# Kernel optimization log

Measured on AMD Instinct MI355X. Metric: run time of the kernel, lower is better.

The kernel has to match this reference:

```python
import jax, jax.numpy as jnp
import numpy as np

B, C, W, H = 2, 64, 96, 96  # N = W*H = 9216 spatial positions


def conv1x1(x, w, b):
    # x: (B, Cin, W, H), w: (Cout, Cin), b: (Cout,) -> (B, Cout, W, H)
    return jnp.einsum('bchw,oc->bohw', x, w) + b[None, :, None, None]


def setup_inputs() -> dict:
    key = jax.random.key(0)
    ks = jax.random.split(key, 4)
    c8 = C // 8
    s = 0.05  # small weight scale keeps softmax logits in a sane range
    return {
        'x': jax.random.normal(ks[0], (B, C, W, H), jnp.float32),
        'wq': jax.random.normal(ks[1], (c8, C), jnp.float32) * s,
        'bq': jnp.zeros((c8,), jnp.float32),
        'wk': jax.random.normal(ks[2], (c8, C), jnp.float32) * s,
        'bk': jnp.zeros((c8,), jnp.float32),
        'wv': jax.random.normal(ks[3], (C, C), jnp.float32) * s,
        'bv': jnp.zeros((C,), jnp.float32),
        'gamma': jnp.full((1,), 0.5, jnp.float32),
    }


def reference(x, wq, bq, wk, bk, wv, bv, gamma):
    b, c, w, h = x.shape
    n = w * h
    q = conv1x1(x, wq, bq).reshape(b, -1, n)   # (B, C//8, N)
    k = conv1x1(x, wk, bk).reshape(b, -1, n)   # (B, C//8, N)
    v = conv1x1(x, wv, bv).reshape(b, c, n)    # (B, C, N)
    energy = jnp.einsum('bci,bcj->bij', q, k)  # (B, N, N)
    attn = jax.nn.softmax(energy, axis=-1)
    # torch.bmm(v, attn): out[b,c,i] = sum_j v[b,c,j] * attn[b,j,i]
    out = jnp.einsum('bcj,bji->bci', v, attn).reshape(b, c, w, h)
    return gamma * out + x
```

## Files before the change

### kernel.cpp

```cpp
#include <hip/hip_runtime.h>

using half2v  = __attribute__((ext_vector_type(2))) _Float16;
using half4   = __attribute__((ext_vector_type(4))) _Float16;
using half8   = __attribute__((ext_vector_type(8))) _Float16;
using floatx4 = __attribute__((ext_vector_type(4))) float;

constexpr int BATCH = 2;
constexpr int NPOS  = 96 * 96;
constexpr int NT    = NPOS / 16;
constexpr int NST   = NPOS / 32;

#define EXP2(x) __builtin_amdgcn_exp2f(x)

__device__ inline half8 p8_of(floatx4 e0, floatx4 e1) {
    half2v a0 = __builtin_bit_cast(half2v,
        __builtin_amdgcn_cvt_pkrtz(EXP2(e0[0]), EXP2(e0[1])));
    half2v a1 = __builtin_bit_cast(half2v,
        __builtin_amdgcn_cvt_pkrtz(EXP2(e0[2]), EXP2(e0[3])));
    half2v a2 = __builtin_bit_cast(half2v,
        __builtin_amdgcn_cvt_pkrtz(EXP2(e1[0]), EXP2(e1[1])));
    half2v a3 = __builtin_bit_cast(half2v,
        __builtin_amdgcn_cvt_pkrtz(EXP2(e1[2]), EXP2(e1[3])));
    half8 p = {a0[0], a0[1], a1[0], a1[1], a2[0], a2[1], a3[0], a3[1]};
    return p;
}

__global__ __launch_bounds__(256) void qkv_kernel(
    const float* __restrict__ x,
    const float* __restrict__ wq, const float* __restrict__ bq,
    const float* __restrict__ wk, const float* __restrict__ bk,
    const float* __restrict__ wv, const float* __restrict__ bv,
    _Float16* __restrict__ Qf, _Float16* __restrict__ Kf,
    _Float16* __restrict__ Vf)
{
    __shared__ float W[80][64];
    __shared__ float bias[80];
    __shared__ float qs[32][8];
    __shared__ float ks[32][8];
    __shared__ _Float16 vs[32][64];
    const int tid = threadIdx.x;
    for (int idx = tid; idx < 80 * 64; idx += 256) {
        int o = idx >> 6, c = idx & 63;
        float w;
        if (o < 8)       w = wq[o * 64 + c];
        else if (o < 16) w = wk[(o - 8) * 64 + c];
        else             w = wv[(o - 16) * 64 + c];
        W[o][c] = w;
    }
    if (tid < 80) {
        float bb;
        if (tid < 8)       bb = bq[tid];
        else if (tid < 16) bb = bk[tid - 8];
        else               bb = bv[tid - 16];
        bias[tid] = bb;
    }
    __syncthreads();

    const int js = blockIdx.x;
    const int b  = blockIdx.y;
    const int part = tid >> 5;
    const int jl   = tid & 31;
    const int i    = js * 32 + jl;

    float xr[64];
    #pragma unroll
    for (int c = 0; c < 64; ++c)
        xr[c] = x[(size_t)(b * 64 + c) * NPOS + i];

    #pragma unroll
    for (int q = 0; q < 10; ++q) {
        const int o = part * 10 + q;
        float s = bias[o];
        #pragma unroll
        for (int c4 = 0; c4 < 16; ++c4) {
            float4 w4 = *(const float4*)&W[o][c4 * 4];
            s += w4.x * xr[c4*4+0] + w4.y * xr[c4*4+1]
               + w4.z * xr[c4*4+2] + w4.w * xr[c4*4+3];
        }
        if (o < 8)       qs[jl][o] = s;
        else if (o < 16) ks[jl][o - 8] = s;
        else             vs[jl][o - 16] = (_Float16)s;
    }
    __syncthreads();

    const size_t tile = (size_t)b * NST + js;
    {
        const int ct = tid >> 6, l = tid & 63;
        const int g = l >> 4, cl = l & 15;
        half8 o8;
        #pragma unroll
        for (int idx = 0; idx < 8; ++idx)
            o8[idx] = vs[8 * g + idx][16 * ct + cl];
        *(half8*)&Vf[(tile * 256 + ct * 64 + l) * 8] = o8;
    }
    if (tid < 128) {
        const int l = tid >> 1, e = tid & 1;
        const int m = l & 15, g = l >> 4;
        const int jsrc = 8 * (m >> 2) + 4 * e + (m & 3);
        constexpr float LOG2E = 1.44269504088896f;
        half4 qh;
        #pragma unroll
        for (int r = 0; r < 4; ++r)
            qh[r] = (g < 2) ? (_Float16)(qs[jsrc][4 * g + r] * LOG2E)
                            : (_Float16)0.f;
        ((half4*)Qf)[(tile * 64 + l) * 2 + e] = qh;
    } else {
        const int t = tid - 128;
        const int ht = t >> 6, l = t & 63;
        const int il = l & 15, g = l >> 4;
        const int it = js * 2 + ht;
        half4 kh;
        #pragma unroll
        for (int r = 0; r < 4; ++r) {
            if (g < 2)       kh[r] = (_Float16)ks[16 * ht + il][4 * g + r];
            else if (g == 2) kh[r] = (r < 2) ? (_Float16)1.f : (_Float16)0.f;
            else             kh[r] = (_Float16)0.f;
        }
        ((half4*)Kf)[(size_t)(b * NT + it) * 64 + l] = kh;
    }
}

__global__ __launch_bounds__(256, 4) void denom_kernel(
    const _Float16* __restrict__ Qf, const _Float16* __restrict__ Kf,
    float* __restrict__ Lp)
{
    __shared__ float LpS[4][64];
    const int tid = threadIdx.x;
    const int w = tid >> 6, l = tid & 63;
    const int jgl = blockIdx.x;
    const int b   = blockIdx.y;
    const int ih  = blockIdx.z;
    const half8* __restrict__ qfb = (const half8*)Qf + (size_t)b * NST * 64;
    const half4* __restrict__ kfb = (const half4*)Kf + (size_t)b * NT * 64;

    half8 qvA = qfb[(size_t)(jgl * 2 + 0) * 64 + l];
    half8 qvB = qfb[(size_t)(jgl * 2 + 1) * 64 + l];
    half4 q0 = __builtin_shufflevector(qvA, qvA, 0, 1, 2, 3);
    half4 q1 = __builtin_shufflevector(qvA, qvA, 4, 5, 6, 7);
    half4 q2 = __builtin_shufflevector(qvB, qvB, 0, 1, 2, 3);
    half4 q3 = __builtin_shufflevector(qvB, qvB, 4, 5, 6, 7);

    float sum[4][4];
    #pragma unroll
    for (int s = 0; s < 4; ++s)
        #pragma unroll
        for (int r = 0; r < 4; ++r) sum[s][r] = 0.f;

    #define DSTEP(KF) do { \
        floatx4 z = {0.f,0.f,0.f,0.f}; \
        floatx4 e0 = __builtin_amdgcn_mfma_f32_16x16x16f16(q0, KF, z, 0,0,0); \
        floatx4 e1 = __builtin_amdgcn_mfma_f32_16x16x16f16(q1, KF, z, 0,0,0); \
        floatx4 e2 = __builtin_amdgcn_mfma_f32_16x16x16f16(q2, KF, z, 0,0,0); \
        floatx4 e3 = __builtin_amdgcn_mfma_f32_16x16x16f16(q3, KF, z, 0,0,0); \
        _Pragma("unroll") \
        for (int r = 0; r < 4; ++r) { \
            sum[0][r] += EXP2(e0[r]); sum[1][r] += EXP2(e1[r]); \
            sum[2][r] += EXP2(e2[r]); sum[3][r] += EXP2(e3[r]); } \
    } while (0)

    const half4* kp = kfb + (size_t)(ih * (NT/2) + w) * 64 + l;
    half4 kf = *kp;
    for (int k = 0; k < 71; ++k) {
        kp += 256;
        half4 kn = *kp;
        DSTEP(kf);
        kf = kn;
    }
    DSTEP(kf);
    #undef DSTEP

    #pragma unroll
    for (int s = 0; s < 4; ++s)
        #pragma unroll
        for (int r = 0; r < 4; ++r)
            #pragma unroll
            for (int m = 1; m < 16; m <<= 1)
                sum[s][r] += __shfl_xor(sum[s][r], m, 64);

    if ((l & 15) == 0) {
        const int g = l >> 4;
        #pragma unroll
        for (int s = 0; s < 4; ++s)
            #pragma unroll
            for (int r = 0; r < 4; ++r)
                LpS[w][(s >> 1) * 32 + 8 * g + 4 * (s & 1) + r] = sum[s][r];
    }
    __syncthreads();
    if (tid < 64) {
        float tot = LpS[0][tid] + LpS[1][tid] + LpS[2][tid] + LpS[3][tid];
        Lp[((size_t)ih * BATCH + b) * NPOS + jgl * 64 + tid] = tot;
    }
}

__global__ __launch_bounds__(256) void patch_kernel(
    const float* __restrict__ Lp, _Float16* __restrict__ Qf)
{
    const int idx = blockIdx.x * 256 + threadIdx.x;
    const int b = idx / NPOS;
    const int j = idx - b * NPOS;
    const float L = Lp[(size_t)b * NPOS + j] + Lp[(size_t)(BATCH + b) * NPOS + j];
    const float v = -__log2f(L);
    _Float16 hi = (_Float16)v;
    _Float16 lo = (_Float16)(v - (float)hi);
    const int js = j >> 5, off = j & 31;
    const int m = ((off >> 3) << 2) | (off & 3);
    const int e = (off >> 2) & 1;
    const size_t tile = (size_t)b * NST + js;
    half2v hl = {hi, lo};
    ((half2v*)Qf)[((tile * 64 + m + 32) * 2 + e) * 2] = hl;
}

__global__ __launch_bounds__(256, 3) void attn_kernel(
    const _Float16* __restrict__ Qf, const _Float16* __restrict__ Kf,
    const _Float16* __restrict__ Vf,
    const float* __restrict__ x, const float* __restrict__ gamma,
    float* __restrict__ out)
{
    __shared__ float red[4][3][64][9];
    const int s = blockIdx.x;
    const int xcd = s & 7;
    const int b   = xcd >> 2;
    const int r2  = (s >> 3) * 4 + (xcd & 3);
    const int igl = r2 % 192;
    const int ch  = r2 / 192;
    const int tid = threadIdx.x;
    const int w = tid >> 6, l = tid & 63;
    const int it0 = igl * 3, i0 = igl * 48;

    const half8* __restrict__ qfb = (const half8*)Qf + (size_t)b * NST * 64;
    const half4* __restrict__ kfb = (const half4*)Kf + (size_t)b * NT * 64;
    const half8* __restrict__ vfb = (const half8*)Vf + (size_t)b * NST * 256;

    half4 kf[3];
    #pragma unroll
    for (int st = 0; st < 3; ++st) kf[st] = kfb[(size_t)(it0 + st) * 64 + l];

    floatx4 acc[3][2];
    #pragma unroll
    for (int st = 0; st < 3; ++st) {
        acc[st][0] = (floatx4){0.f, 0.f, 0.f, 0.f};
        acc[st][1] = (floatx4){0.f, 0.f, 0.f, 0.f};
    }

    #define ASTEP(QV, V0, V1) do { \
        half4 qe0 = __builtin_shufflevector(QV, QV, 0, 1, 2, 3); \
        half4 qe1 = __builtin_shufflevector(QV, QV, 4, 5, 6, 7); \
        floatx4 z = {0.f,0.f,0.f,0.f}; \
        _Pragma("unroll") \
        for (int st = 0; st < 3; ++st) { \
            floatx4 e0 = __builtin_amdgcn_mfma_f32_16x16x16f16(qe0, kf[st], z, 0,0,0); \
            floatx4 e1 = __builtin_amdgcn_mfma_f32_16x16x16f16(qe1, kf[st], z, 0,0,0); \
            half8 p = p8_of(e0, e1); \
            acc[st][0] = __builtin_amdgcn_mfma_f32_16x16x32_f16(V0, p, acc[st][0], 0,0,0); \
            acc[st][1] = __builtin_amdgcn_mfma_f32_16x16x32_f16(V1, p, acc[st][1], 0,0,0); \
        } \
    } while (0)

    const half8* qp = qfb + (size_t)w * 64 + l;
    const half8* vp = vfb + (size_t)w * 256 + ch * 128 + l;
    half8 qv = *qp;
    half8 v0 = vp[0], v1 = vp[64];
    for (int k = 0; k < 71; ++k) {
        qp += 256; vp += 1024;
        half8 qn  = *qp;
        half8 v0n = vp[0], v1n = vp[64];
        ASTEP(qv, v0, v1);
        qv = qn; v0 = v0n; v1 = v1n;
    }
    ASTEP(qv, v0, v1);
    #undef ASTEP

    #pragma unroll
    for (int st = 0; st < 3; ++st)
        #pragma unroll
        for (int t2 = 0; t2 < 2; ++t2)
            #pragma unroll
            for (int r = 0; r < 4; ++r)
                red[w][st][l][t2 * 4 + r] = acc[st][t2][r];
    __syncthreads();

    if (w < 3) {
        const float g = gamma[0];
        const int iq = i0 + 16 * w + (l & 15);
        #pragma unroll
        for (int t2 = 0; t2 < 2; ++t2)
            #pragma unroll
            for (int r = 0; r < 4; ++r) {
                float v = red[0][w][l][t2*4+r] + red[1][w][l][t2*4+r]
                        + red[2][w][l][t2*4+r] + red[3][w][l][t2*4+r];
                int c = 16 * (2 * ch + t2) + 4 * (l >> 4) + r;
                size_t o = ((size_t)(b * 64 + c)) * NPOS + iq;
                out[o] = g * v + x[o];
            }
    }
}

extern "C" void kernel_launch(void* const* d_in, const int* in_sizes, int n_in,
                              void* d_out, int out_size, void* d_ws, size_t ws_size,
                              hipStream_t stream)
{
    const float* x     = (const float*)d_in[0];
    const float* wq    = (const float*)d_in[1];
    const float* bq    = (const float*)d_in[2];
    const float* wk    = (const float*)d_in[3];
    const float* bk    = (const float*)d_in[4];
    const float* wv    = (const float*)d_in[5];
    const float* bv    = (const float*)d_in[6];
    const float* gamma = (const float*)d_in[7];
    float* out = (float*)d_out;

    char* wsb = (char*)d_ws;
    _Float16* Qf = (_Float16*)wsb;
    _Float16* Kf = (_Float16*)(wsb + 589824);
    _Float16* Vf = (_Float16*)(wsb + 1179648);
    float*    Lp = (float*)(wsb + 3538944);

    qkv_kernel<<<dim3(NST, BATCH), 256, 0, stream>>>(
        x, wq, bq, wk, bk, wv, bv, Qf, Kf, Vf);

    denom_kernel<<<dim3(NST / 2, BATCH, 2), 256, 0, stream>>>(Qf, Kf, Lp);

    patch_kernel<<<dim3(BATCH * NPOS / 256), 256, 0, stream>>>(Lp, Qf);

    attn_kernel<<<dim3(768), 256, 0, stream>>>(Qf, Kf, Vf, x, gamma, out);
}
```

Before: 150.2 us.

## Fuse four kernels into one persistent kernel with grid-wide barriers

Merges the QKV projection, softmax-denominator, log-patch and attention kernels into a single 768-block launch. The stages are separated by atomic-counter grid barriers in workspace memory, which is zeroed by a memset before each launch. The aim is to remove the launch gaps and tail effects between the four kernels. The cost is barrier spin overhead. It also depends on all 768 blocks being co-resident (256 CUs × 4 occupancy bound = 1024 slots, 44KB of LDS per block), otherwise the barriers deadlock. Launch bounds also change from 3 to 4 blocks for the attention phase.

```diff
diff --git a/kernel.cpp b/kernel.cpp
--- a/kernel.cpp
+++ b/kernel.cpp
@@ -9,6 +9,7 @@
 constexpr int NPOS  = 96 * 96;
 constexpr int NT    = NPOS / 16;
 constexpr int NST   = NPOS / 32;
+constexpr int GRID  = 768;
 
 #define EXP2(x) __builtin_amdgcn_exp2f(x)
 
@@ -25,273 +26,288 @@
     return p;
 }
 
-__global__ __launch_bounds__(256) void qkv_kernel(
+__device__ inline void gbar(unsigned* bar, int slot) {
+    __syncthreads();
+    if (threadIdx.x == 0) {
+        __threadfence();
+        __hip_atomic_fetch_add(bar + slot, 1u,
+                               __ATOMIC_ACQ_REL, __HIP_MEMORY_SCOPE_AGENT);
+        while (__hip_atomic_load(bar + slot,
+                                 __ATOMIC_ACQUIRE, __HIP_MEMORY_SCOPE_AGENT)
+               < (unsigned)GRID)
+            __builtin_amdgcn_s_sleep(8);
+    }
+    __syncthreads();
+}
+
+__global__ __launch_bounds__(256, 4) void fused_kernel(
     const float* __restrict__ x,
     const float* __restrict__ wq, const float* __restrict__ bq,
     const float* __restrict__ wk, const float* __restrict__ bk,
     const float* __restrict__ wv, const float* __restrict__ bv,
+    const float* __restrict__ gamma,
     _Float16* __restrict__ Qf, _Float16* __restrict__ Kf,
-    _Float16* __restrict__ Vf)
+    _Float16* __restrict__ Vf, float* __restrict__ Lp,
+    unsigned* __restrict__ bar, float* __restrict__ out)
 {
-    __shared__ float W[80][64];
-    __shared__ float bias[80];
-    __shared__ float qs[32][8];
-    __shared__ float ks[32][8];
-    __shared__ _Float16 vs[32][64];
+    __shared__ __align__(16) char smem[44032];
+    const int bi  = blockIdx.x;
     const int tid = threadIdx.x;
-    for (int idx = tid; idx < 80 * 64; idx += 256) {
-        int o = idx >> 6, c = idx & 63;
-        float w;
-        if (o < 8)       w = wq[o * 64 + c];
-        else if (o < 16) w = wk[(o - 8) * 64 + c];
-        else             w = wv[(o - 16) * 64 + c];
-        W[o][c] = w;
-    }
-    if (tid < 80) {
-        float bb;
-        if (tid < 8)       bb = bq[tid];
-        else if (tid < 16) bb = bk[tid - 8];
-        else               bb = bv[tid - 16];
-        bias[tid] = bb;
-    }
-    __syncthreads();
-
-    const int js = blockIdx.x;
-    const int b  = blockIdx.y;
-    const int part = tid >> 5;
-    const int jl   = tid & 31;
-    const int i    = js * 32 + jl;
-
-    float xr[64];
-    #pragma unroll
-    for (int c = 0; c < 64; ++c)
-        xr[c] = x[(size_t)(b * 64 + c) * NPOS + i];
-
-    #pragma unroll
-    for (int q = 0; q < 10; ++q) {
-        const int o = part * 10 + q;
-        float s = bias[o];
-        #pragma unroll
-        for (int c4 = 0; c4 < 16; ++c4) {
-            float4 w4 = *(const float4*)&W[o][c4 * 4];
-            s += w4.x * xr[c4*4+0] + w4.y * xr[c4*4+1]
-               + w4.z * xr[c4*4+2] + w4.w * xr[c4*4+3];
-        }
-        if (o < 8)       qs[jl][o] = s;
-        else if (o < 16) ks[jl][o - 8] = s;
-        else             vs[jl][o - 16] = (_Float16)s;
-    }
-    __syncthreads();
-
-    const size_t tile = (size_t)b * NST + js;
+
+    if (bi < 576) {
+        float (*W)[64]      = (float (*)[64])smem;
+        float* bias         = (float*)(smem + 20480);
+        float (*qs)[8]      = (float (*)[8])(smem + 20800);
+        float (*ks)[8]      = (float (*)[8])(smem + 21824);
+        _Float16 (*vs)[64]  = (_Float16 (*)[64])(smem + 22848);
+
+        for (int idx = tid; idx < 80 * 64; idx += 256) {
+            int o = idx >> 6, c = idx & 63;
+            float w;
+            if (o < 8)       w = wq[o * 64 + c];
+            else if (o < 16) w = wk[(o - 8) * 64 + c];
+            else             w = wv[(o - 16) * 64 + c];
+            W[o][c] = w;
+        }
+        if (tid < 80) {
+            float bb;
+            if (tid < 8)       bb = bq[tid];
+            else if (tid < 16) bb = bk[tid - 8];
+            else               bb = bv[tid - 16];
+            bias[tid] = bb;
+        }
+        __syncthreads();
+
+        const int js = bi % NST;
+        const int b  = bi / NST;
+        const int part = tid >> 5;
+        const int jl   = tid & 31;
+        const int i    = js * 32 + jl;
+
+        float xr[64];
+        #pragma unroll
+        for (int c = 0; c < 64; ++c)
+            xr[c] = x[(size_t)(b * 64 + c) * NPOS + i];
+
+        #pragma unroll
+        for (int q = 0; q < 10; ++q) {
+            const int o = part * 10 + q;
+            float s = bias[o];
+            #pragma unroll
+            for (int c4 = 0; c4 < 16; ++c4) {
+                float4 w4 = *(const float4*)&W[o][c4 * 4];
+                s += w4.x * xr[c4*4+0] + w4.y * xr[c4*4+1]
+                   + w4.z * xr[c4*4+2] + w4.w * xr[c4*4+3];
+            }
+            if (o < 8)       qs[jl][o] = s;
+            else if (o < 16) ks[jl][o - 8] = s;
+            else             vs[jl][o - 16] = (_Float16)s;
+        }
+        __syncthreads();
+
+        const size_t tile = (size_t)b * NST + js;
+        {
+            const int ct = tid >> 6, l = tid & 63;
+            const int g = l >> 4, cl = l & 15;
+            half8 o8;
+            #pragma unroll
+            for (int idx = 0; idx < 8; ++idx)
+                o8[idx] = vs[8 * g + idx][16 * ct + cl];
+            *(half8*)&Vf[(tile * 256 + ct * 64 + l) * 8] = o8;
+        }
+        if (tid < 128) {
+            const int l = tid >> 1, e = tid & 1;
+            const int m = l & 15, g = l >> 4;
+            const int jsrc = 8 * (m >> 2) + 4 * e + (m & 3);
+            constexpr float LOG2E = 1.44269504088896f;
+            half4 qh;
+            #pragma unroll
+            for (int r = 0; r < 4; ++r)
+                qh[r] = (g < 2) ? (_Float16)(qs[jsrc][4 * g + r] * LOG2E)
+                                : (_Float16)0.f;
+            ((half4*)Qf)[(tile * 64 + l) * 2 + e] = qh;
+        } else {
+            const int t = tid - 128;
+            const int ht = t >> 6, l = t & 63;
+            const int il = l & 15, g = l >> 4;
+            const int it = js * 2 + ht;
+            half4 kh;
+            #pragma unroll
+            for (int r = 0; r < 4; ++r) {
+                if (g < 2)       kh[r] = (_Float16)ks[16 * ht + il][4 * g + r];
+                else if (g == 2) kh[r] = (r < 2) ? (_Float16)1.f : (_Float16)0.f;
+                else             kh[r] = (_Float16)0.f;
+            }
+            ((half4*)Kf)[(size_t)(b * NT + it) * 64 + l] = kh;
+        }
+    }
+    gbar(bar, 0);
+
+    if (bi < 576) {
+        float (*LpS)[64] = (float (*)[64])smem;
+        const int w = tid >> 6, l = tid & 63;
+        const int jgl = bi % 144;
+        const int rem = bi / 144;
+        const int b   = rem & 1;
+        const int ih  = rem >> 1;
+        const half8* __restrict__ qfb = (const half8*)Qf + (size_t)b * NST * 64;
+        const half4* __restrict__ kfb = (const half4*)Kf + (size_t)b * NT * 64;
+
+        half8 qvA = qfb[(size_t)(jgl * 2 + 0) * 64 + l];
+        half8 qvB = qfb[(size_t)(jgl * 2 + 1) * 64 + l];
+        half4 q0 = __builtin_shufflevector(qvA, qvA, 0, 1, 2, 3);
+        half4 q1 = __builtin_shufflevector(qvA, qvA, 4, 5, 6, 7);
+        half4 q2 = __builtin_shufflevector(qvB, qvB, 0, 1, 2, 3);
+        half4 q3 = __builtin_shufflevector(qvB, qvB, 4, 5, 6, 7);
+
+        float sum[4][4];
+        #pragma unroll
+        for (int s = 0; s < 4; ++s)
+            #pragma unroll
+            for (int r = 0; r < 4; ++r) sum[s][r] = 0.f;
+
+        #define DSTEP(KF) do { \
+            floatx4 z = {0.f,0.f,0.f,0.f}; \
+            floatx4 e0 = __builtin_amdgcn_mfma_f32_16x16x16f16(q0, KF, z, 0,0,0); \
+            floatx4 e1 = __builtin_amdgcn_mfma_f32_16x16x16f16(q1, KF, z, 0,0,0); \
+            floatx4 e2 = __builtin_amdgcn_mfma_f32_16x16x16f16(q2, KF, z, 0,0,0); \
+            floatx4 e3 = __builtin_amdgcn_mfma_f32_16x16x16f16(q3, KF, z, 0,0,0); \
+            _Pragma("unroll") \
+            for (int r = 0; r < 4; ++r) { \
+                sum[0][r] += EXP2(e0[r]); sum[1][r] += EXP2(e1[r]); \
+                sum[2][r] += EXP2(e2[r]); sum[3][r] += EXP2(e3[r]); } \
+        } while (0)
+
+        const half4* kp = kfb + (size_t)(ih * (NT/2) + w) * 64 + l;
+        half4 kf = *kp;
+        for (int k = 0; k < 71; ++k) {
+            kp += 256;
+            half4 kn = *kp;
+            DSTEP(kf);
+            kf = kn;
+        }
+        DSTEP(kf);
+        #undef DSTEP
+
+        #pragma unroll
+        for (int s = 0; s < 4; ++s)
+            #pragma unroll
+            for (int r = 0; r < 4; ++r)
+                #pragma unroll
+                for (int m = 1; m < 16; m <<= 1)
+                    sum[s][r] += __shfl_xor(sum[s][r], m, 64);
+
+        if ((l & 15) == 0) {
+            const int g = l >> 4;
+            #pragma unroll
+            for (int s = 0; s < 4; ++s)
+                #pragma unroll
+                for (int r = 0; r < 4; ++r)
+                    LpS[w][(s >> 1) * 32 + 8 * g + 4 * (s & 1) + r] = sum[s][r];
+        }
+        __syncthreads();
+        if (tid < 64) {
+            float tot = LpS[0][tid] + LpS[1][tid] + LpS[2][tid] + LpS[3][tid];
+            Lp[((size_t)ih * BATCH + b) * NPOS + jgl * 64 + tid] = tot;
+        }
+    }
+    gbar(bar, 1);
+
+    if (bi < 72) {
+        const int idx = bi * 256 + tid;
+        const int b = idx / NPOS;
+        const int j = idx - b * NPOS;
+        const float L = Lp[(size_t)b * NPOS + j]
+                      + Lp[(size_t)(BATCH + b) * NPOS + j];
+        const float v = -__log2f(L);
+        _Float16 hi = (_Float16)v;
+        _Float16 lo = (_Float16)(v - (float)hi);
+        const int js = j >> 5, off = j & 31;
+        const int m = ((off >> 3) << 2) | (off & 3);
+        const int e = (off >> 2) & 1;
+        const size_t tile = (size_t)b * NST + js;
+        half2v hl = {hi, lo};
+        ((half2v*)Qf)[((tile * 64 + m + 32) * 2 + e) * 2] = hl;
+    }
+    gbar(bar, 2);
+
     {
-        const int ct = tid >> 6, l = tid & 63;
-        const int g = l >> 4, cl = l & 15;
-        half8 o8;
-        #pragma unroll
-        for (int idx = 0; idx < 8; ++idx)
-            o8[idx] = vs[8 * g + idx][16 * ct + cl];
-        *(half8*)&Vf[(tile * 256 + ct * 64 + l) * 8] = o8;
-    }
-    if (tid < 128) {
-        const int l = tid >> 1, e = tid & 1;
-        const int m = l & 15, g = l >> 4;
-        const int jsrc = 8 * (m >> 2) + 4 * e + (m & 3);
-        constexpr float LOG2E = 1.44269504088896f;
-        half4 qh;
-        #pragma unroll
-        for (int r = 0; r < 4; ++r)
-            qh[r] = (g < 2) ? (_Float16)(qs[jsrc][4 * g + r] * LOG2E)
-                            : (_Float16)0.f;
-        ((half4*)Qf)[(tile * 64 + l) * 2 + e] = qh;
-    } else {
-        const int t = tid - 128;
-        const int ht = t >> 6, l = t & 63;
-        const int il = l & 15, g = l >> 4;
-        const int it = js * 2 + ht;
-        half4 kh;
-        #pragma unroll
-        for (int r = 0; r < 4; ++r) {
-            if (g < 2)       kh[r] = (_Float16)ks[16 * ht + il][4 * g + r];
-            else if (g == 2) kh[r] = (r < 2) ? (_Float16)1.f : (_Float16)0.f;
-            else             kh[r] = (_Float16)0.f;
-        }
-        ((half4*)Kf)[(size_t)(b * NT + it) * 64 + l] = kh;
-    }
-}
-
-__global__ __launch_bounds__(256, 4) void denom_kernel(
-    const _Float16* __restrict__ Qf, const _Float16* __restrict__ Kf,
-    float* __restrict__ Lp)
-{
-    __shared__ float LpS[4][64];
-    const int tid = threadIdx.x;
-    const int w = tid >> 6, l = tid & 63;
-    const int jgl = blockIdx.x;
-    const int b   = blockIdx.y;
-    const int ih  = blockIdx.z;
-    const half8* __restrict__ qfb = (const half8*)Qf + (size_t)b * NST * 64;
-    const half4* __restrict__ kfb = (const half4*)Kf + (size_t)b * NT * 64;
-
-    half8 qvA = qfb[(size_t)(jgl * 2 + 0) * 64 + l];
-    half8 qvB = qfb[(size_t)(jgl * 2 + 1) * 64 + l];
-    half4 q0 = __builtin_shufflevector(qvA, qvA, 0, 1, 2, 3);
-    half4 q1 = __builtin_shufflevector(qvA, qvA, 4, 5, 6, 7);
-    half4 q2 = __builtin_shufflevector(qvB, qvB, 0, 1, 2, 3);
-    half4 q3 = __builtin_shufflevector(qvB, qvB, 4, 5, 6, 7);
-
-    float sum[4][4];
-    #pragma unroll
-    for (int s = 0; s < 4; ++s)
-        #pragma unroll
-        for (int r = 0; r < 4; ++r) sum[s][r] = 0.f;
-
-    #define DSTEP(KF) do { \
-        floatx4 z = {0.f,0.f,0.f,0.f}; \
-        floatx4 e0 = __builtin_amdgcn_mfma_f32_16x16x16f16(q0, KF, z, 0,0,0); \
-        floatx4 e1 = __builtin_amdgcn_mfma_f32_16x16x16f16(q1, KF, z, 0,0,0); \
-        floatx4 e2 = __builtin_amdgcn_mfma_f32_16x16x16f16(q2, KF, z, 0,0,0); \
-        floatx4 e3 = __builtin_amdgcn_mfma_f32_16x16x16f16(q3, KF, z, 0,0,0); \
-        _Pragma("unroll") \
-        for (int r = 0; r < 4; ++r) { \
-            sum[0][r] += EXP2(e0[r]); sum[1][r] += EXP2(e1[r]); \
-            sum[2][r] += EXP2(e2[r]); sum[3][r] += EXP2(e3[r]); } \
-    } while (0)
-
-    const half4* kp = kfb + (size_t)(ih * (NT/2) + w) * 64 + l;
-    half4 kf = *kp;
-    for (int k = 0; k < 71; ++k) {
-        kp += 256;
-        half4 kn = *kp;
-        DSTEP(kf);
-        kf = kn;
-    }
-    DSTEP(kf);
-    #undef DSTEP
-
-    #pragma unroll
-    for (int s = 0; s < 4; ++s)
-        #pragma unroll
-        for (int r = 0; r < 4; ++r)
-            #pragma unroll
-            for (int m = 1; m < 16; m <<= 1)
-                sum[s][r] += __shfl_xor(sum[s][r], m, 64);
-
-    if ((l & 15) == 0) {
-        const int g = l >> 4;
-        #pragma unroll
-        for (int s = 0; s < 4; ++s)
-            #pragma unroll
-            for (int r = 0; r < 4; ++r)
-                LpS[w][(s >> 1) * 32 + 8 * g + 4 * (s & 1) + r] = sum[s][r];
-    }
-    __syncthreads();
-    if (tid < 64) {
-        float tot = LpS[0][tid] + LpS[1][tid] + LpS[2][tid] + LpS[3][tid];
-        Lp[((size_t)ih * BATCH + b) * NPOS + jgl * 64 + tid] = tot;
-    }
-}
-
-__global__ __launch_bounds__(256) void patch_kernel(
-    const float* __restrict__ Lp, _Float16* __restrict__ Qf)
-{
-    const int idx = blockIdx.x * 256 + threadIdx.x;
-    const int b = idx / NPOS;
-    const int j = idx - b * NPOS;
-    const float L = Lp[(size_t)b * NPOS + j] + Lp[(size_t)(BATCH + b) * NPOS + j];
-    const float v = -__log2f(L);
-    _Float16 hi = (_Float16)v;
-    _Float16 lo = (_Float16)(v - (float)hi);
-    const int js = j >> 5, off = j & 31;
-    const int m = ((off >> 3) << 2) | (off & 3);
-    const int e = (off >> 2) & 1;
-    const size_t tile = (size_t)b * NST + js;
-    half2v hl = {hi, lo};
-    ((half2v*)Qf)[((tile * 64 + m + 32) * 2 + e) * 2] = hl;
-}
-
-__global__ __launch_bounds__(256, 3) void attn_kernel(
-    const _Float16* __restrict__ Qf, const _Float16* __restrict__ Kf,
-    const _Float16* __restrict__ Vf,
-    const float* __restrict__ x, const float* __restrict__ gamma,
-    float* __restrict__ out)
-{
-    __shared__ float red[4][3][64][9];
-    const int s = blockIdx.x;
-    const int xcd = s & 7;
-    const int b   = xcd >> 2;
-    const int r2  = (s >> 3) * 4 + (xcd & 3);
-    const int igl = r2 % 192;
-    const int ch  = r2 / 192;
-    const int tid = threadIdx.x;
-    const int w = tid >> 6, l = tid & 63;
-    const int it0 = igl * 3, i0 = igl * 48;
-
-    const half8* __restrict__ qfb = (const half8*)Qf + (size_t)b * NST * 64;
-    const half4* __restrict__ kfb = (const half4*)Kf + (size_t)b * NT * 64;
-    const half8* __restrict__ vfb = (const half8*)Vf + (size_t)b * NST * 256;
-
-    half4 kf[3];
-    #pragma unroll
-    for (int st = 0; st < 3; ++st) kf[st] = kfb[(size_t)(it0 + st) * 64 + l];
-
-    floatx4 acc[3][2];
-    #pragma unroll
-    for (int st = 0; st < 3; ++st) {
-        acc[st][0] = (floatx4){0.f, 0.f, 0.f, 0.f};
-        acc[st][1] = (floatx4){0.f, 0.f, 0.f, 0.f};
-    }
-
-    #define ASTEP(QV, V0, V1) do { \
-        half4 qe0 = __builtin_shufflevector(QV, QV, 0, 1, 2, 3); \
-        half4 qe1 = __builtin_shufflevector(QV, QV, 4, 5, 6, 7); \
-        floatx4 z = {0.f,0.f,0.f,0.f}; \
-        _Pragma("unroll") \
-        for (int st = 0; st < 3; ++st) { \
-            floatx4 e0 = __builtin_amdgcn_mfma_f32_16x16x16f16(qe0, kf[st], z, 0,0,0); \
-            floatx4 e1 = __builtin_amdgcn_mfma_f32_16x16x16f16(qe1, kf[st], z, 0,0,0); \
-            half8 p = p8_of(e0, e1); \
-            acc[st][0] = __builtin_amdgcn_mfma_f32_16x16x32_f16(V0, p, acc[st][0], 0,0,0); \
-            acc[st][1] = __builtin_amdgcn_mfma_f32_16x16x32_f16(V1, p, acc[st][1], 0,0,0); \
-        } \
-    } while (0)
-
-    const half8* qp = qfb + (size_t)w * 64 + l;
-    const half8* vp = vfb + (size_t)w * 256 + ch * 128 + l;
-    half8 qv = *qp;
-    half8 v0 = vp[0], v1 = vp[64];
-    for (int k = 0; k < 71; ++k) {
-        qp += 256; vp += 1024;
-        half8 qn  = *qp;
-        half8 v0n = vp[0], v1n = vp[64];
+        float (*red)[3][64][9] = (float (*)[3][64][9])smem;
+        const int s = bi;
+        const int xcd = s & 7;
+        const int b   = xcd >> 2;
+        const int r2  = (s >> 3) * 4 + (xcd & 3);
+        const int igl = r2 % 192;
+        const int ch  = r2 / 192;
+        const int w = tid >> 6, l = tid & 63;
+        const int it0 = igl * 3, i0 = igl * 48;
+
+        const half8* __restrict__ qfb = (const half8*)Qf + (size_t)b * NST * 64;
+        const half4* __restrict__ kfb = (const half4*)Kf + (size_t)b * NT * 64;
+        const half8* __restrict__ vfb = (const half8*)Vf + (size_t)b * NST * 256;
+
+        half4 kf[3];
+        #pragma unroll
+        for (int st = 0; st < 3; ++st) kf[st] = kfb[(size_t)(it0 + st) * 64 + l];
+
+        floatx4 acc[3][2];
+        #pragma unroll
+        for (int st = 0; st < 3; ++st) {
+            acc[st][0] = (floatx4){0.f, 0.f, 0.f, 0.f};
+            acc[st][1] = (floatx4){0.f, 0.f, 0.f, 0.f};
+        }
+
+        #define ASTEP(QV, V0, V1) do { \
+            half4 qe0 = __builtin_shufflevector(QV, QV, 0, 1, 2, 3); \
+            half4 qe1 = __builtin_shufflevector(QV, QV, 4, 5, 6, 7); \
+            floatx4 z = {0.f,0.f,0.f,0.f}; \
+            _Pragma("unroll") \
+            for (int st = 0; st < 3; ++st) { \
+                floatx4 e0 = __builtin_amdgcn_mfma_f32_16x16x16f16(qe0, kf[st], z, 0,0,0); \
+                floatx4 e1 = __builtin_amdgcn_mfma_f32_16x16x16f16(qe1, kf[st], z, 0,0,0); \
+                half8 p = p8_of(e0, e1); \
+                acc[st][0] = __builtin_amdgcn_mfma_f32_16x16x32_f16(V0, p, acc[st][0], 0,0,0); \
+                acc[st][1] = __builtin_amdgcn_mfma_f32_16x16x32_f16(V1, p, acc[st][1], 0,0,0); \
+            } \
+        } while (0)
+
+        const half8* qp = qfb + (size_t)w * 64 + l;
+        const half8* vp = vfb + (size_t)w * 256 + ch * 128 + l;
+        half8 qv = *qp;
+        half8 v0 = vp[0], v1 = vp[64];
+        for (int k = 0; k < 71; ++k) {
+            qp += 256; vp += 1024;
+            half8 qn  = *qp;
+            half8 v0n = vp[0], v1n = vp[64];
+            ASTEP(qv, v0, v1);
+            qv = qn; v0 = v0n; v1 = v1n;
+        }
         ASTEP(qv, v0, v1);
-        qv = qn; v0 = v0n; v1 = v1n;
-    }
-    ASTEP(qv, v0, v1);
-    #undef ASTEP
-
-    #pragma unroll
-    for (int st = 0; st < 3; ++st)
-        #pragma unroll
-        for (int t2 = 0; t2 < 2; ++t2)
-            #pragma unroll
-            for (int r = 0; r < 4; ++r)
-                red[w][st][l][t2 * 4 + r] = acc[st][t2][r];
-    __syncthreads();
-
-    if (w < 3) {
-        const float g = gamma[0];
-        const int iq = i0 + 16 * w + (l & 15);
-        #pragma unroll
-        for (int t2 = 0; t2 < 2; ++t2)
-            #pragma unroll
-            for (int r = 0; r < 4; ++r) {
-                float v = red[0][w][l][t2*4+r] + red[1][w][l][t2*4+r]
-                        + red[2][w][l][t2*4+r] + red[3][w][l][t2*4+r];
-                int c = 16 * (2 * ch + t2) + 4 * (l >> 4) + r;
-                size_t o = ((size_t)(b * 64 + c)) * NPOS + iq;
-                out[o] = g * v + x[o];
-            }
+        #undef ASTEP
+
+        #pragma unroll
+        for (int st = 0; st < 3; ++st)
+            #pragma unroll
+            for (int t2 = 0; t2 < 2; ++t2)
+                #pragma unroll
+                for (int r = 0; r < 4; ++r)
+                    red[w][st][l][t2 * 4 + r] = acc[st][t2][r];
+        __syncthreads();
+
+        if (w < 3) {
+            const float g = gamma[0];
+            const int iq = i0 + 16 * w + (l & 15);
+            #pragma unroll
+            for (int t2 = 0; t2 < 2; ++t2)
+                #pragma unroll
+                for (int r = 0; r < 4; ++r) {
+                    float v = red[0][w][l][t2*4+r] + red[1][w][l][t2*4+r]
+                            + red[2][w][l][t2*4+r] + red[3][w][l][t2*4+r];
+                    int c = 16 * (2 * ch + t2) + 4 * (l >> 4) + r;
+                    size_t o = ((size_t)(b * 64 + c)) * NPOS + iq;
+                    out[o] = g * v + x[o];
+                }
+        }
     }
 }
 
@@ -310,17 +326,14 @@
     float* out = (float*)d_out;
 
     char* wsb = (char*)d_ws;
-    _Float16* Qf = (_Float16*)wsb;
-    _Float16* Kf = (_Float16*)(wsb + 589824);
-    _Float16* Vf = (_Float16*)(wsb + 1179648);
-    float*    Lp = (float*)(wsb + 3538944);
-
-    qkv_kernel<<<dim3(NST, BATCH), 256, 0, stream>>>(
-        x, wq, bq, wk, bk, wv, bv, Qf, Kf, Vf);
-
-    denom_kernel<<<dim3(NST / 2, BATCH, 2), 256, 0, stream>>>(Qf, Kf, Lp);
-
-    patch_kernel<<<dim3(BATCH * NPOS / 256), 256, 0, stream>>>(Lp, Qf);
-
-    attn_kernel<<<dim3(768), 256, 0, stream>>>(Qf, Kf, Vf, x, gamma, out);
+    _Float16* Qf  = (_Float16*)wsb;
+    _Float16* Kf  = (_Float16*)(wsb + 589824);
+    _Float16* Vf  = (_Float16*)(wsb + 1179648);
+    float*    Lp  = (float*)(wsb + 3538944);
+    unsigned* bar = (unsigned*)(wsb + 3686400);
+
+    hipMemsetAsync(bar, 0, 128, stream);
+
+    fused_kernel<<<dim3(GRID), 256, 0, stream>>>(
+        x, wq, bq, wk, bk, wv, bv, gamma, Qf, Kf, Vf, Lp, bar, out);
 }
```

After: 386.8 us. +157.5%, slower.

## Fuse denominator patching into denom kernel and software-pipeline attention loops

Applied to the files above, without the earlier changes.

The denom kernel now has each block cover one 32-row query tile over all keys. It computes the log-denominator and writes the hi/lo correction into Qf directly, which removes the patch kernel, the Lp buffer and one launch. The denom and attn main loops become two-stage ping-pong pipelines, so the score MFMAs for the next step are issued while exp and PV MFMAs of the current step run. Shared-memory arrays in the QKV kernel are padded to reduce bank conflicts. The cost is higher register pressure in attn from the doubled score and V buffers, which could lower occupancy.

```diff
diff --git a/kernel.cpp b/kernel.cpp
--- a/kernel.cpp
+++ b/kernel.cpp
@@ -11,6 +11,8 @@
 constexpr int NST   = NPOS / 32;
 
 #define EXP2(x) __builtin_amdgcn_exp2f(x)
+#define MFMA16(A, B, C) __builtin_amdgcn_mfma_f32_16x16x16f16(A, B, C, 0, 0, 0)
+#define MFMA32(A, B, C) __builtin_amdgcn_mfma_f32_16x16x32_f16(A, B, C, 0, 0, 0)
 
 __device__ inline half8 p8_of(floatx4 e0, floatx4 e1) {
     half2v a0 = __builtin_bit_cast(half2v,
@@ -35,9 +37,9 @@
 {
     __shared__ float W[80][64];
     __shared__ float bias[80];
-    __shared__ float qs[32][8];
-    __shared__ float ks[32][8];
-    __shared__ _Float16 vs[32][64];
+    __shared__ float qs[32][9];
+    __shared__ float ks[32][9];
+    __shared__ _Float16 vs[32][72];
     const int tid = threadIdx.x;
     for (int idx = tid; idx < 80 * 64; idx += 256) {
         int o = idx >> 6, c = idx & 63;
@@ -121,93 +123,81 @@
 }
 
 __global__ __launch_bounds__(256, 4) void denom_kernel(
-    const _Float16* __restrict__ Qf, const _Float16* __restrict__ Kf,
-    float* __restrict__ Lp)
+    _Float16* __restrict__ Qf, const _Float16* __restrict__ Kf)
 {
-    __shared__ float LpS[4][64];
+    __shared__ float LpS[4][32];
     const int tid = threadIdx.x;
     const int w = tid >> 6, l = tid & 63;
-    const int jgl = blockIdx.x;
-    const int b   = blockIdx.y;
-    const int ih  = blockIdx.z;
+    const int js = blockIdx.x;
+    const int b  = blockIdx.y;
+    const size_t tile = (size_t)b * NST + js;
     const half8* __restrict__ qfb = (const half8*)Qf + (size_t)b * NST * 64;
     const half4* __restrict__ kfb = (const half4*)Kf + (size_t)b * NT * 64;
 
-    half8 qvA = qfb[(size_t)(jgl * 2 + 0) * 64 + l];
-    half8 qvB = qfb[(size_t)(jgl * 2 + 1) * 64 + l];
-    half4 q0 = __builtin_shufflevector(qvA, qvA, 0, 1, 2, 3);
-    half4 q1 = __builtin_shufflevector(qvA, qvA, 4, 5, 6, 7);
-    half4 q2 = __builtin_shufflevector(qvB, qvB, 0, 1, 2, 3);
-    half4 q3 = __builtin_shufflevector(qvB, qvB, 4, 5, 6, 7);
-
-    float sum[4][4];
-    #pragma unroll
-    for (int s = 0; s < 4; ++s)
-        #pragma unroll
-        for (int r = 0; r < 4; ++r) sum[s][r] = 0.f;
-
-    #define DSTEP(KF) do { \
-        floatx4 z = {0.f,0.f,0.f,0.f}; \
-        floatx4 e0 = __builtin_amdgcn_mfma_f32_16x16x16f16(q0, KF, z, 0,0,0); \
-        floatx4 e1 = __builtin_amdgcn_mfma_f32_16x16x16f16(q1, KF, z, 0,0,0); \
-        floatx4 e2 = __builtin_amdgcn_mfma_f32_16x16x16f16(q2, KF, z, 0,0,0); \
-        floatx4 e3 = __builtin_amdgcn_mfma_f32_16x16x16f16(q3, KF, z, 0,0,0); \
+    half8 qv = qfb[tile % ((size_t)NST) * 64 + ((size_t)0) + js * 0 + (size_t)js * 64 - (size_t)js * 64 + (size_t)js * 64 + l];
+    qv = qfb[(size_t)js * 64 + l];
+    half4 q0 = __builtin_shufflevector(qv, qv, 0, 1, 2, 3);
+    half4 q1 = __builtin_shufflevector(qv, qv, 4, 5, 6, 7);
+
+    float sum[2][4];
+    #pragma unroll
+    for (int e = 0; e < 2; ++e)
+        #pragma unroll
+        for (int r = 0; r < 4; ++r) sum[e][r] = 0.f;
+
+    const floatx4 z = {0.f, 0.f, 0.f, 0.f};
+    #define DACC(E0, E1) do { \
         _Pragma("unroll") \
         for (int r = 0; r < 4; ++r) { \
-            sum[0][r] += EXP2(e0[r]); sum[1][r] += EXP2(e1[r]); \
-            sum[2][r] += EXP2(e2[r]); sum[3][r] += EXP2(e3[r]); } \
+            sum[0][r] += EXP2(E0[r]); sum[1][r] += EXP2(E1[r]); } \
     } while (0)
 
-    const half4* kp = kfb + (size_t)(ih * (NT/2) + w) * 64 + l;
-    half4 kf = *kp;
+    const half4* kp = kfb + (size_t)w * 64 + l;
+    half4 kfA = kp[0];
+    half4 kfB = kp[256];
+    floatx4 eA0 = MFMA16(q0, kfA, z), eA1 = MFMA16(q1, kfA, z);
+    floatx4 eB0, eB1;
     for (int k = 0; k < 71; ++k) {
-        kp += 256;
-        half4 kn = *kp;
-        DSTEP(kf);
-        kf = kn;
-    }
-    DSTEP(kf);
-    #undef DSTEP
-
-    #pragma unroll
-    for (int s = 0; s < 4; ++s)
+        kfA = kp[(size_t)(2 * k + 2) * 256];
+        eB0 = MFMA16(q0, kfB, z); eB1 = MFMA16(q1, kfB, z);
+        DACC(eA0, eA1);
+        kfB = kp[(size_t)(2 * k + 3) * 256];
+        eA0 = MFMA16(q0, kfA, z); eA1 = MFMA16(q1, kfA, z);
+        DACC(eB0, eB1);
+    }
+    eB0 = MFMA16(q0, kfB, z); eB1 = MFMA16(q1, kfB, z);
+    DACC(eA0, eA1);
+    DACC(eB0, eB1);
+    #undef DACC
+
+    #pragma unroll
+    for (int e = 0; e < 2; ++e)
         #pragma unroll
         for (int r = 0; r < 4; ++r)
             #pragma unroll
             for (int m = 1; m < 16; m <<= 1)
-                sum[s][r] += __shfl_xor(sum[s][r], m, 64);
+                sum[e][r] += __shfl_xor(sum[e][r], m, 64);
 
     if ((l & 15) == 0) {
         const int g = l >> 4;
         #pragma unroll
-        for (int s = 0; s < 4; ++s)
+        for (int e = 0; e < 2; ++e)
             #pragma unroll
             for (int r = 0; r < 4; ++r)
-                LpS[w][(s >> 1) * 32 + 8 * g + 4 * (s & 1) + r] = sum[s][r];
+                LpS[w][8 * g + 4 * e + r] = sum[e][r];
     }
     __syncthreads();
-    if (tid < 64) {
-        float tot = LpS[0][tid] + LpS[1][tid] + LpS[2][tid] + LpS[3][tid];
-        Lp[((size_t)ih * BATCH + b) * NPOS + jgl * 64 + tid] = tot;
-    }
-}
-
-__global__ __launch_bounds__(256) void patch_kernel(
-    const float* __restrict__ Lp, _Float16* __restrict__ Qf)
-{
-    const int idx = blockIdx.x * 256 + threadIdx.x;
-    const int b = idx / NPOS;
-    const int j = idx - b * NPOS;
-    const float L = Lp[(size_t)b * NPOS + j] + Lp[(size_t)(BATCH + b) * NPOS + j];
-    const float v = -__log2f(L);
-    _Float16 hi = (_Float16)v;
-    _Float16 lo = (_Float16)(v - (float)hi);
-    const int js = j >> 5, off = j & 31;
-    const int m = ((off >> 3) << 2) | (off & 3);
-    const int e = (off >> 2) & 1;
-    const size_t tile = (size_t)b * NST + js;
-    half2v hl = {hi, lo};
-    ((half2v*)Qf)[((tile * 64 + m + 32) * 2 + e) * 2] = hl;
+
+    if (tid < 32) {
+        const float L = LpS[0][tid] + LpS[1][tid] + LpS[2][tid] + LpS[3][tid];
+        const float v = -__log2f(L);
+        _Float16 hi = (_Float16)v;
+        _Float16 lo = (_Float16)(v - (float)hi);
+        const int m = 4 * (tid >> 3) + (tid & 3);
+        const int e = (tid >> 2) & 1;
+        half2v hl = {hi, lo};
+        ((half2v*)Qf)[((tile * 64 + m + 32) * 2 + e) * 2] = hl;
+    }
 }
 
 __global__ __launch_bounds__(256, 3) void attn_kernel(
@@ -242,33 +232,54 @@
         acc[st][1] = (floatx4){0.f, 0.f, 0.f, 0.f};
     }
 
-    #define ASTEP(QV, V0, V1) do { \
+    const floatx4 z = {0.f, 0.f, 0.f, 0.f};
+
+    #define E_STEP(QV, E) do { \
         half4 qe0 = __builtin_shufflevector(QV, QV, 0, 1, 2, 3); \
         half4 qe1 = __builtin_shufflevector(QV, QV, 4, 5, 6, 7); \
-        floatx4 z = {0.f,0.f,0.f,0.f}; \
-        _Pragma("unroll") \
-        for (int st = 0; st < 3; ++st) { \
-            floatx4 e0 = __builtin_amdgcn_mfma_f32_16x16x16f16(qe0, kf[st], z, 0,0,0); \
-            floatx4 e1 = __builtin_amdgcn_mfma_f32_16x16x16f16(qe1, kf[st], z, 0,0,0); \
-            half8 p = p8_of(e0, e1); \
-            acc[st][0] = __builtin_amdgcn_mfma_f32_16x16x32_f16(V0, p, acc[st][0], 0,0,0); \
-            acc[st][1] = __builtin_amdgcn_mfma_f32_16x16x32_f16(V1, p, acc[st][1], 0,0,0); \
-        } \
+        E[0] = MFMA16(qe0, kf[0], z); E[1] = MFMA16(qe1, kf[0], z); \
+        E[2] = MFMA16(qe0, kf[1], z); E[3] = MFMA16(qe1, kf[1], z); \
+        E[4] = MFMA16(qe0, kf[2], z); E[5] = MFMA16(qe1, kf[2], z); \
     } while (0)
 
-    const half8* qp = qfb + (size_t)w * 64 + l;
-    const half8* vp = vfb + (size_t)w * 256 + ch * 128 + l;
-    half8 qv = *qp;
-    half8 v0 = vp[0], v1 = vp[64];
-    for (int k = 0; k < 71; ++k) {
-        qp += 256; vp += 1024;
-        half8 qn  = *qp;
-        half8 v0n = vp[0], v1n = vp[64];
-        ASTEP(qv, v0, v1);
-        qv = qn; v0 = v0n; v1 = v1n;
-    }
-    ASTEP(qv, v0, v1);
-    #undef ASTEP
+    #define PXV(E, V0, V1) do { \
+        half8 p0 = p8_of(E[0], E[1]); \
+        half8 p1 = p8_of(E[2], E[3]); \
+        half8 p2 = p8_of(E[4], E[5]); \
+        acc[0][0] = MFMA32(V0, p0, acc[0][0]); \
+        acc[0][1] = MFMA32(V1, p0, acc[0][1]); \
+        acc[1][0] = MFMA32(V0, p1, acc[1][0]); \
+        acc[1][1] = MFMA32(V1, p1, acc[1][1]); \
+        acc[2][0] = MFMA32(V0, p2, acc[2][0]); \
+        acc[2][1] = MFMA32(V1, p2, acc[2][1]); \
+    } while (0)
+
+    const half8* qpw = qfb + (size_t)w * 64 + l;
+    const half8* vpw = vfb + (size_t)w * 256 + ch * 128 + l;
+
+    floatx4 eA[6], eB[6];
+    half8 qvA = qpw[0];
+    half8 v0A = vpw[0],    v1A = vpw[64];
+    half8 qvB = qpw[256];
+    half8 v0B = vpw[1024], v1B = vpw[1024 + 64];
+    E_STEP(qvA, eA);
+
+    for (int k = 0; k < 35; ++k) {
+        const size_t s2 = (size_t)(2 * k + 2), s3 = (size_t)(2 * k + 3);
+        qvA = qpw[s2 * 256];
+        E_STEP(qvB, eB);
+        PXV(eA, v0A, v1A);
+        v0A = vpw[s2 * 1024]; v1A = vpw[s2 * 1024 + 64];
+        qvB = qpw[s3 * 256];
+        E_STEP(qvA, eA);
+        PXV(eB, v0B, v1B);
+        v0B = vpw[s3 * 1024]; v1B = vpw[s3 * 1024 + 64];
+    }
+    E_STEP(qvB, eB);
+    PXV(eA, v0A, v1A);
+    PXV(eB, v0B, v1B);
+    #undef E_STEP
+    #undef PXV
 
     #pragma unroll
     for (int st = 0; st < 3; ++st)
@@ -313,14 +324,11 @@
     _Float16* Qf = (_Float16*)wsb;
     _Float16* Kf = (_Float16*)(wsb + 589824);
     _Float16* Vf = (_Float16*)(wsb + 1179648);
-    float*    Lp = (float*)(wsb + 3538944);
 
     qkv_kernel<<<dim3(NST, BATCH), 256, 0, stream>>>(
         x, wq, bq, wk, bk, wv, bv, Qf, Kf, Vf);
 
-    denom_kernel<<<dim3(NST / 2, BATCH, 2), 256, 0, stream>>>(Qf, Kf, Lp);
-
-    patch_kernel<<<dim3(BATCH * NPOS / 256), 256, 0, stream>>>(Lp, Qf);
+    denom_kernel<<<dim3(NST, BATCH), 256, 0, stream>>>(Qf, Kf);
 
     attn_kernel<<<dim3(768), 256, 0, stream>>>(Qf, Kf, Vf, x, gamma, out);
 }
```

Result: faster. 144.8 us (-3.6%).
